# Optimization experiments

Measured on AMD Instinct MI355X. Metric: run time of the kernel, lower is better.

The kernel has to match this reference:

```python
import jax, jax.numpy as jnp
import numpy as np

T, H, W = 16, 14, 14
C = 512          # embed_dim
DS = 7           # down_size (divides H and W exactly)
B = 64


def setup_inputs() -> dict:
    key = jax.random.key(0)
    x_in = jax.random.normal(key, (B, C, T, H * W), dtype=jnp.float32)
    return {"x_in": x_in}


def reference(x_in):
    b, c, t, hw = x_in.shape
    k = T // 2
    scaler = 1.0 / C

    # (b, c, t, hw) -> (b, T, C, H, W)
    xi = x_in.reshape(b, C, T, H, W).transpose(0, 2, 1, 3, 4)
    # adaptive_avg_pool2d 14->7 with exact divisibility == mean over 2x2 blocks
    xi = xi.reshape(b, T, C, DS, H // DS, DS, W // DS).mean(axis=(4, 6))  # (b,T,C,7,7)
    # permute to (b, T, 7, 7, C) then flatten frame features
    xi = xi.transpose(0, 1, 3, 4, 2).reshape(b, T, DS * DS * C)
    # scaled dot similarity between frames, then mean over keys -> (b, T)
    sim = jnp.einsum('btd,bsd->bts', scaler * xi, xi)
    score = sim.mean(axis=-1)
    # prior bias [1,0,1,0,...] favoring even frames as 'approx'
    prior = jnp.tile(jnp.array([1.0, 0.0], dtype=score.dtype), t // 2)
    score = score + prior[None, :]

    _, approx_index = jax.lax.top_k(score, k)    # largest
    _, detail_index = jax.lax.top_k(-score, k)   # smallest
    approx_index = jnp.sort(approx_index, axis=-1)
    detail_index = jnp.sort(detail_index, axis=-1)

    # gather frames along time: (b, t, c, hw)
    xt = x_in.transpose(0, 2, 1, 3)
    x_a = jnp.take_along_axis(xt, approx_index[:, :, None, None], axis=1)
    x_d = jnp.take_along_axis(xt, detail_index[:, :, None, None], axis=1)
    # back to (b, c, k, hw)
    return (x_a.transpose(0, 2, 1, 3), x_d.transpose(0, 2, 1, 3))
```

## Files before the change

kernel.cpp:

```cpp
#include <hip/hip_runtime.h>

#define B_ 64
#define C_ 512
#define T_ 16
#define HW_ 196
#define K_ 8
#define D_ 49

__global__ void zero_scores(float* __restrict__ score) {
    score[threadIdx.x] = 0.0f;
}

__global__ __launch_bounds__(256) void pool_score_kernel(const float* __restrict__ x,
                                                         float* __restrict__ score) {
    __shared__ float tile[T_ * HW_];
    __shared__ float pool[T_ * D_];
    __shared__ float ysum[D_];

    const unsigned bc = blockIdx.x;
    const unsigned b  = bc >> 9;
    const int tid = threadIdx.x;

    const float4* src4 = (const float4*)(x + (size_t)bc * (T_ * HW_));
    float4* tile4 = (float4*)tile;
    for (int i = tid; i < T_ * HW_ / 4; i += 256) tile4[i] = src4[i];
    __syncthreads();

    for (int i = tid; i < T_ * D_; i += 256) {
        int t  = i / 49;
        int pq = i - t * 49;
        int p  = pq / 7;
        int q  = pq - p * 7;
        int base = t * 196 + p * 28 + q * 2;
        pool[i] = 0.25f * (tile[base] + tile[base + 1] + tile[base + 14] + tile[base + 15]);
    }
    __syncthreads();

    if (tid < D_) {
        float s = 0.0f;
        for (int t = 0; t < T_; ++t) s += pool[t * 49 + tid];
        ysum[tid] = s;
    }
    __syncthreads();

    if (tid < T_) {
        float acc = 0.0f;
        for (int pq = 0; pq < 49; ++pq) acc += pool[tid * 49 + pq] * ysum[pq];
        atomicAdd(&score[b * T_ + tid], acc);
    }
}

__global__ void select_kernel(const float* __restrict__ score, int* __restrict__ sel) {
    __shared__ float fs[B_ * T_];
    const int tid = threadIdx.x;
    const int b = tid >> 4;
    const int t = tid & 15;
    float v = score[tid] * (1.0f / (C_ * T_)) + ((t & 1) ? 0.0f : 1.0f);
    fs[tid] = v;
    __syncthreads();

    const float* S = fs + b * T_;
    bool memA[T_], memD[T_];
    for (int s = 0; s < T_; ++s) {
        int rd = 0, ra = 0;
        float vs = S[s];
        for (int u = 0; u < T_; ++u) {
            float vu = S[u];
            rd += (vu > vs) || (vu == vs && u < s);
            ra += (vu < vs) || (vu == vs && u < s);
        }
        memA[s] = rd < K_;
        memD[s] = ra < K_;
    }
    if (memA[t]) {
        int pos = 0;
        for (int s = 0; s < t; ++s) pos += memA[s];
        sel[b * T_ + pos] = t;
    }
    if (memD[t]) {
        int pos = 0;
        for (int s = 0; s < t; ++s) pos += memD[s];
        sel[b * T_ + K_ + pos] = t;
    }
}

__global__ __launch_bounds__(256) void gather_kernel(const float* __restrict__ x,
                                                     const int* __restrict__ sel,
                                                     float* __restrict__ out) {
    const unsigned idx = blockIdx.x * 256u + threadIdx.x;
    const unsigned q   = idx % 49u;
    const unsigned row = idx / 49u;
    const unsigned j   = row & 15u;
    const unsigned bc  = row >> 4;
    const unsigned b   = bc >> 9;

    const int t = sel[b * T_ + j];
    const float4* src = (const float4*)x + (size_t)(bc * T_ + t) * (HW_ / 4) + q;

    const unsigned halfOff = (unsigned)B_ * C_ * K_ * (HW_ / 4);
    float4* o4 = (float4*)out;
    unsigned dst = (j < K_)
        ? ((bc * K_ + j) * (HW_ / 4) + q)
        : (halfOff + (bc * K_ + (j - K_)) * (HW_ / 4) + q);
    o4[dst] = *src;
}

extern "C" void kernel_launch(void* const* d_in, const int* in_sizes, int n_in,
                              void* d_out, int out_size, void* d_ws, size_t ws_size,
                              hipStream_t stream) {
    const float* x = (const float*)d_in[0];
    float* out = (float*)d_out;
    float* score = (float*)d_ws;
    int*   sel   = (int*)((char*)d_ws + 4096);

    zero_scores<<<1, B_ * T_, 0, stream>>>(score);
    pool_score_kernel<<<B_ * C_, 256, 0, stream>>>(x, score);
    select_kernel<<<1, B_ * T_, 0, stream>>>(score, sel);
    gather_kernel<<<(B_ * C_ * T_ * 49) / 256, 256, 0, stream>>>(x, sel, out);
}
```

Before: 768.7 us.

## Replace atomic score accumulation with per-channel partials and parallel per-batch selection

The pool-score kernel now writes per-(b,c) partial frame scores to workspace instead of doing atomicAdds, and a new 64-block select kernel reduces those partials and ranks frames with ballot/popcount. This drops the zero kernel, the contention from atomics on 1024 addresses, and the serial single-block selection. The per-frame dot product is also spread over 16 lanes with shuffle reduction. A fallback path with channel-grouped atomics is used when the workspace is too small, so which path runs depends on ws_size.

```diff
diff --git a/kernel.cpp b/kernel.cpp
--- a/kernel.cpp
+++ b/kernel.cpp
@@ -6,19 +6,16 @@
 #define HW_ 196
 #define K_ 8
 #define D_ 49
-
-__global__ void zero_scores(float* __restrict__ score) {
-    score[threadIdx.x] = 0.0f;
-}
+#define G_ 8
+
 
 __global__ __launch_bounds__(256) void pool_score_kernel(const float* __restrict__ x,
-                                                         float* __restrict__ score) {
+                                                         float* __restrict__ partial) {
     __shared__ float tile[T_ * HW_];
     __shared__ float pool[T_ * D_];
     __shared__ float ysum[D_];
 
     const unsigned bc = blockIdx.x;
-    const unsigned b  = bc >> 9;
     const int tid = threadIdx.x;
 
     const float4* src4 = (const float4*)(x + (size_t)bc * (T_ * HW_));
@@ -38,19 +35,126 @@
 
     if (tid < D_) {
         float s = 0.0f;
+        #pragma unroll
         for (int t = 0; t < T_; ++t) s += pool[t * 49 + tid];
         ysum[tid] = s;
     }
     __syncthreads();
 
+    const int t = tid >> 4;
+    const int l = tid & 15;
+    float acc = 0.0f;
+    for (int pq = l; pq < D_; pq += 16) acc += pool[t * 49 + pq] * ysum[pq];
+    acc += __shfl_xor(acc, 8);
+    acc += __shfl_xor(acc, 4);
+    acc += __shfl_xor(acc, 2);
+    acc += __shfl_xor(acc, 1);
+    if (l == 0) partial[(size_t)bc * T_ + t] = acc;
+}
+
+__global__ __launch_bounds__(256) void select_kernel_A(const float* __restrict__ partial,
+                                                       int* __restrict__ sel) {
+    __shared__ float part[256];
+    __shared__ float S[T_];
+    const int b = blockIdx.x;
+    const int tid = threadIdx.x;
+    const int t  = tid & 15;
+    const int cg = tid >> 4;
+
+    const float* P = partial + (size_t)b * C_ * T_;
+    float s = 0.0f;
+    for (int c = cg * 32; c < cg * 32 + 32; ++c) s += P[c * T_ + t];
+    part[tid] = s;
+    __syncthreads();
+
     if (tid < T_) {
+        float tot = 0.0f;
+        #pragma unroll
+        for (int g = 0; g < 16; ++g) tot += part[g * 16 + tid];
+        S[tid] = tot * (1.0f / (C_ * T_)) + ((tid & 1) ? 0.0f : 1.0f);
+    }
+    __syncthreads();
+
+    if (tid < T_) {
+        float vs = S[tid];
+        int rd = 0, ra = 0;
+        #pragma unroll
+        for (int u = 0; u < T_; ++u) {
+            float vu = S[u];
+            rd += (vu > vs) || (vu == vs && u < tid);
+            ra += (vu < vs) || (vu == vs && u < tid);
+        }
+        bool memA = rd < K_;
+        bool memD = ra < K_;
+        unsigned long long mA = __ballot(memA);
+        unsigned long long mD = __ballot(memD);
+        int posA = __popcll(mA & ((1ull << tid) - 1));
+        int posD = __popcll(mD & ((1ull << tid) - 1));
+        if (memA) sel[b * T_ + posA] = tid;
+        if (memD) sel[b * T_ + K_ + posD] = tid;
+    }
+}
+
+
+__global__ void zero_scores(float* __restrict__ score) {
+    score[threadIdx.x] = 0.0f;
+}
+
+__global__ __launch_bounds__(256) void pool_score_atomic_kernel(const float* __restrict__ x,
+                                                                float* __restrict__ score) {
+    __shared__ float tile[T_ * HW_];
+    __shared__ float pool[T_ * D_];
+    __shared__ float ysum[D_];
+    __shared__ float sacc[T_];
+
+    const unsigned blk = blockIdx.x;
+    const unsigned b   = blk / (C_ / G_);
+    const unsigned cg  = blk % (C_ / G_);
+    const int tid = threadIdx.x;
+
+    if (tid < T_) sacc[tid] = 0.0f;
+
+    for (int ci = 0; ci < G_; ++ci) {
+        __syncthreads();
+        const unsigned bc = b * C_ + cg * G_ + ci;
+        const float4* src4 = (const float4*)(x + (size_t)bc * (T_ * HW_));
+        float4* tile4 = (float4*)tile;
+        for (int i = tid; i < T_ * HW_ / 4; i += 256) tile4[i] = src4[i];
+        __syncthreads();
+
+        for (int i = tid; i < T_ * D_; i += 256) {
+            int t  = i / 49;
+            int pq = i - t * 49;
+            int p  = pq / 7;
+            int q  = pq - p * 7;
+            int base = t * 196 + p * 28 + q * 2;
+            pool[i] = 0.25f * (tile[base] + tile[base + 1] + tile[base + 14] + tile[base + 15]);
+        }
+        __syncthreads();
+
+        if (tid < D_) {
+            float s = 0.0f;
+            #pragma unroll
+            for (int t = 0; t < T_; ++t) s += pool[t * 49 + tid];
+            ysum[tid] = s;
+        }
+        __syncthreads();
+
+        const int t = tid >> 4;
+        const int l = tid & 15;
         float acc = 0.0f;
-        for (int pq = 0; pq < 49; ++pq) acc += pool[tid * 49 + pq] * ysum[pq];
-        atomicAdd(&score[b * T_ + tid], acc);
-    }
-}
-
-__global__ void select_kernel(const float* __restrict__ score, int* __restrict__ sel) {
+        for (int pq = l; pq < D_; pq += 16) acc += pool[t * 49 + pq] * ysum[pq];
+        acc += __shfl_xor(acc, 8);
+        acc += __shfl_xor(acc, 4);
+        acc += __shfl_xor(acc, 2);
+        acc += __shfl_xor(acc, 1);
+        if (l == 0) sacc[t] += acc;
+    }
+    __syncthreads();
+    if (tid < T_) atomicAdd(&score[b * T_ + tid], sacc[tid]);
+}
+
+__global__ void select_kernel_B(const float* __restrict__ score, int* __restrict__ sel) {
     __shared__ float fs[B_ * T_];
     const int tid = threadIdx.x;
     const int b = tid >> 4;
@@ -60,26 +164,42 @@
     __syncthreads();
 
     const float* S = fs + b * T_;
-    bool memA[T_], memD[T_];
-    for (int s = 0; s < T_; ++s) {
-        int rd = 0, ra = 0;
-        float vs = S[s];
+    float vs = S[t];
+    int rd = 0, ra = 0;
+    bool memA_t, memD_t;
+    {
         for (int u = 0; u < T_; ++u) {
             float vu = S[u];
-            rd += (vu > vs) || (vu == vs && u < s);
-            ra += (vu < vs) || (vu == vs && u < s);
-        }
-        memA[s] = rd < K_;
-        memD[s] = ra < K_;
-    }
-    if (memA[t]) {
+            rd += (vu > vs) || (vu == vs && u < t);
+            ra += (vu < vs) || (vu == vs && u < t);
+        }
+        memA_t = rd < K_;
+        memD_t = ra < K_;
+    }
+    if (memA_t) {
         int pos = 0;
-        for (int s = 0; s < t; ++s) pos += memA[s];
+        for (int s = 0; s < t; ++s) {
+            float vu = S[s];
+            int r = 0;
+            for (int u = 0; u < T_; ++u) {
+                float vv = S[u];
+                r += (vv > vu) || (vv == vu && u < s);
+            }
+            pos += (r < K_);
+        }
         sel[b * T_ + pos] = t;
     }
-    if (memD[t]) {
+    if (memD_t) {
         int pos = 0;
-        for (int s = 0; s < t; ++s) pos += memD[s];
+        for (int s = 0; s < t; ++s) {
+            float vu = S[s];
+            int r = 0;
+            for (int u = 0; u < T_; ++u) {
+                float vv = S[u];
+                r += (vv < vu) || (vv == vu && u < s);
+            }
+            pos += (r < K_);
+        }
         sel[b * T_ + K_ + pos] = t;
     }
 }
@@ -110,11 +230,21 @@
                               hipStream_t stream) {
     const float* x = (const float*)d_in[0];
     float* out = (float*)d_out;
-    float* score = (float*)d_ws;
-    int*   sel   = (int*)((char*)d_ws + 4096);
-
-    zero_scores<<<1, B_ * T_, 0, stream>>>(score);
-    pool_score_kernel<<<B_ * C_, 256, 0, stream>>>(x, score);
-    select_kernel<<<1, B_ * T_, 0, stream>>>(score, sel);
-    gather_kernel<<<(B_ * C_ * T_ * 49) / 256, 256, 0, stream>>>(x, sel, out);
-}
+
+    const size_t partialBytes = (size_t)B_ * C_ * T_ * sizeof(float);
+
+    if (ws_size >= partialBytes + 4096) {
+        float* partial = (float*)d_ws;
+        int*   sel     = (int*)((char*)d_ws + partialBytes);
+        pool_score_kernel<<<B_ * C_, 256, 0, stream>>>(x, partial);
+        select_kernel_A<<<B_, 256, 0, stream>>>(partial, sel);
+        gather_kernel<<<(B_ * C_ * T_ * 49) / 256, 256, 0, stream>>>(x, sel, out);
+    } else {
+        float* score = (float*)d_ws;
+        int*   sel   = (int*)((char*)d_ws + 4096);
+        zero_scores<<<1, B_ * T_, 0, stream>>>(score);
+        pool_score_atomic_kernel<<<B_ * (C_ / G_), 256, 0, stream>>>(x, score);
+        select_kernel_B<<<1, B_ * T_, 0, stream>>>(score, sel);
+        gather_kernel<<<(B_ * C_ * T_ * 49) / 256, 256, 0, stream>>>(x, sel, out);
+    }
+}
```

Measured after the change: 729.1 us. -5.1%, faster.
